# Kernel optimization log

Hardware: AMD Instinct MI355X
Metric: run time of the kernel (lower is better)

## Reference

```python
import jax, jax.numpy as jnp
import numpy as np


def setup_inputs() -> dict:
    key = jax.random.key(0)
    x = jax.random.normal(key, (2, 192, 360, 720), dtype=jnp.float32)
    return {"x": x, "pad_width": 3}


def reference(x, pad_width):
    # x: [B, C, H, W]; geo-cyclic padding:
    #  - circular (periodic) padding of width pad_width in longitude (last axis)
    #  - polar wrap: top/bottom halo rows are rows reflected across the pole,
    #    shifted by half the longitude circle (W // 2).
    B, C, H, W = x.shape
    p = pad_width
    # Circular longitude padding: [B, C, H, W + 2p]
    cp = jnp.concatenate([x[:, :, :, -p:], x, x[:, :, :, :p]], axis=3)
    mid = W // 2
    # Each halo row is cat(row[mid:], row[:mid]) == roll by -mid along longitude.
    rolled = jnp.roll(cp, -mid, axis=3)
    i = np.arange(p)
    top_rows = (p - i - 1) % H          # rows written at output rows 0..p-1
    bottom_rows = (H - i - 1) % H       # rows written at output rows H+p..H+2p-1
    top = rolled[:, :, top_rows, :]     # [B, C, p, W+2p]
    bottom = rolled[:, :, bottom_rows, :]
    # Output: [B, C, H + 2p, W + 2p]
    return jnp.concatenate([top, cp, bottom], axis=2)
```

## Files before the change

kernel.cpp:

```cpp
#include <hip/hip_runtime.h>


typedef float f4u __attribute__((ext_vector_type(4), aligned(4)));
typedef float f2u __attribute__((ext_vector_type(2), aligned(8)));

__global__ __launch_bounds__(256) void geo_pad_kernel(const float* __restrict__ x,
                                                      float* __restrict__ out) {
    constexpr int W = 720, H = 360, p = 3, Wp = 726, Hp = 366;
    constexpr int TPR = 182;

    const unsigned t = blockIdx.x * 256u + threadIdx.x;
    const unsigned row = t / TPR;
    const int j = (int)(t - row * TPR);
    const int ho = (int)(row % Hp);
    const int bc = (int)(row / Hp);

    const bool mid = (ho >= p) & (ho < p + H);
    const int h = mid ? (ho - p) : ((ho < p) ? (p - 1 - ho) : (2 * H + p - 1 - ho));
    const int off = mid ? 0 : (W / 2);

    const float* __restrict__ srow = x + ((size_t)bc * H + h) * W;
    float* __restrict__ orow = out + (size_t)row * Wp;

    if (j < TPR - 1) {
        const int wp0 = 4 * j;
        int wr0 = wp0 + off;      if (wr0 >= Wp) wr0 -= Wp;
        int wr3 = wp0 + 3 + off;  if (wr3 >= Wp) wr3 -= Wp;
        int w0 = wr0 - p; if (w0 < 0) w0 += W; else if (w0 >= W) w0 -= W;
        int w3 = wr3 - p; if (w3 < 0) w3 += W; else if (w3 >= W) w3 -= W;

        float v0, v1, v2, v3;
        if (w3 == w0 + 3) {
            f4u tmp = __builtin_nontemporal_load(
                reinterpret_cast<const f4u*>(srow + w0));
            v0 = tmp.x; v1 = tmp.y; v2 = tmp.z; v3 = tmp.w;
        } else {
            int wr1 = wp0 + 1 + off; if (wr1 >= Wp) wr1 -= Wp;
            int wr2 = wp0 + 2 + off; if (wr2 >= Wp) wr2 -= Wp;
            int w1 = wr1 - p; if (w1 < 0) w1 += W; else if (w1 >= W) w1 -= W;
            int w2 = wr2 - p; if (w2 < 0) w2 += W; else if (w2 >= W) w2 -= W;
            v0 = srow[w0]; v1 = srow[w1]; v2 = srow[w2]; v3 = srow[w3];
        }
        f4u sv; sv.x = v0; sv.y = v1; sv.z = v2; sv.w = v3;
        __builtin_nontemporal_store(sv, reinterpret_cast<f4u*>(orow + wp0));
    } else {
        int wr0 = 724 + off; if (wr0 >= Wp) wr0 -= Wp;
        int w0 = wr0 - p; if (w0 < 0) w0 += W; else if (w0 >= W) w0 -= W;
        f2u sv; sv.x = srow[w0]; sv.y = srow[w0 + 1];
        __builtin_nontemporal_store(sv, reinterpret_cast<f2u*>(orow + 724));
    }
}

extern "C" void kernel_launch(void* const* d_in, const int* in_sizes, int n_in,
                              void* d_out, int out_size, void* d_ws, size_t ws_size,
                              hipStream_t stream) {
    const float* x = (const float*)d_in[0];
    float* out = (float*)d_out;

    const unsigned total = 384u * 366u * 182u;
    const unsigned block = 256;
    const unsigned grid = total / block;

    geo_pad_kernel<<<grid, block, 0, stream>>>(x, out);
}
```

Before: 147.3 us.

## Split padding into aligned-input bulk copy and scalar halo pass

The kernel now maps bulk threads to input rows, so every thread does a 16-byte-aligned vector load of four floats and stores them, offset by the pad, into the interior of the output. A separate set of threads writes the left and right column halos and the polar halo rows one float at a time. This removes the per-thread wrap-around index arithmetic and the scalar fallback path from the interior copy. In exchange, the vector stores are always misaligned, because of the 3-column offset and the 726-float row stride, and the halos use scalar, non-coalesced-friendly accesses.

```diff
diff --git a/kernel.cpp b/kernel.cpp
--- a/kernel.cpp
+++ b/kernel.cpp
@@ -1,53 +1,57 @@
 #include <hip/hip_runtime.h>
 
 
+typedef float f4a __attribute__((ext_vector_type(4), aligned(16)));
 typedef float f4u __attribute__((ext_vector_type(4), aligned(4)));
-typedef float f2u __attribute__((ext_vector_type(2), aligned(8)));
 
 __global__ __launch_bounds__(256) void geo_pad_kernel(const float* __restrict__ x,
                                                       float* __restrict__ out) {
     constexpr int W = 720, H = 360, p = 3, Wp = 726, Hp = 366;
-    constexpr int TPR = 182;
+    constexpr unsigned BULK = 384u * 360u * 180u;
+    constexpr unsigned EPP  = 360u * 6u + 6u * 726u;
 
     const unsigned t = blockIdx.x * 256u + threadIdx.x;
-    const unsigned row = t / TPR;
-    const int j = (int)(t - row * TPR);
-    const int ho = (int)(row % Hp);
-    const int bc = (int)(row / Hp);
 
-    const bool mid = (ho >= p) & (ho < p + H);
-    const int h = mid ? (ho - p) : ((ho < p) ? (p - 1 - ho) : (2 * H + p - 1 - ho));
-    const int off = mid ? 0 : (W / 2);
+    if (t < BULK) {
+        const unsigned k  = t % 180u;
+        const unsigned rr = t / 180u;
+        const unsigned r  = rr % 360u;
+        const unsigned bc = rr / 360u;
 
-    const float* __restrict__ srow = x + ((size_t)bc * H + h) * W;
-    float* __restrict__ orow = out + (size_t)row * Wp;
+        const f4a* src = reinterpret_cast<const f4a*>(
+            x + (size_t)(bc * 360u + r) * W) + k;
+        f4a v = __builtin_nontemporal_load(src);
 
-    if (j < TPR - 1) {
-        const int wp0 = 4 * j;
-        int wr0 = wp0 + off;      if (wr0 >= Wp) wr0 -= Wp;
-        int wr3 = wp0 + 3 + off;  if (wr3 >= Wp) wr3 -= Wp;
-        int w0 = wr0 - p; if (w0 < 0) w0 += W; else if (w0 >= W) w0 -= W;
-        int w3 = wr3 - p; if (w3 < 0) w3 += W; else if (w3 >= W) w3 -= W;
+        float* dst = out + ((size_t)bc * Hp + (r + 3)) * Wp + 3 + 4 * k;
+        f4u sv;
+        sv.x = v.x; sv.y = v.y; sv.z = v.z; sv.w = v.w;
+        __builtin_nontemporal_store(sv, reinterpret_cast<f4u*>(dst));
+    } else {
+        const unsigned e  = t - BULK;
+        const unsigned bc = e / EPP;
+        const unsigned q  = e % EPP;
 
-        float v0, v1, v2, v3;
-        if (w3 == w0 + 3) {
-            f4u tmp = __builtin_nontemporal_load(
-                reinterpret_cast<const f4u*>(srow + w0));
-            v0 = tmp.x; v1 = tmp.y; v2 = tmp.z; v3 = tmp.w;
+        int ho, col, h, w;
+        if (q < 2160u) {
+            const int r  = (int)(q / 6u);
+            const int c6 = (int)(q % 6u);
+            ho  = r + p;
+            h   = r;
+            col = (c6 < 3) ? c6 : (720 + c6);
+            w   = (c6 < 3) ? (717 + c6) : (c6 - 3);
         } else {
-            int wr1 = wp0 + 1 + off; if (wr1 >= Wp) wr1 -= Wp;
-            int wr2 = wp0 + 2 + off; if (wr2 >= Wp) wr2 -= Wp;
-            int w1 = wr1 - p; if (w1 < 0) w1 += W; else if (w1 >= W) w1 -= W;
-            int w2 = wr2 - p; if (w2 < 0) w2 += W; else if (w2 >= W) w2 -= W;
-            v0 = srow[w0]; v1 = srow[w1]; v2 = srow[w2]; v3 = srow[w3];
+            const unsigned q2 = q - 2160u;
+            const int hr = (int)(q2 / (unsigned)Wp);
+            col = (int)(q2 % (unsigned)Wp);
+            ho  = (hr < p) ? hr : (H + hr);
+            h   = (hr < p) ? (p - 1 - hr) : (362 - hr);
+            int wr = col + W / 2;
+            if (wr >= Wp) wr -= Wp;
+            w = wr - p;
+            if (w < 0) w += W; else if (w >= W) w -= W;
         }
-        f4u sv; sv.x = v0; sv.y = v1; sv.z = v2; sv.w = v3;
-        __builtin_nontemporal_store(sv, reinterpret_cast<f4u*>(orow + wp0));
-    } else {
-        int wr0 = 724 + off; if (wr0 >= Wp) wr0 -= Wp;
-        int w0 = wr0 - p; if (w0 < 0) w0 += W; else if (w0 >= W) w0 -= W;
-        f2u sv; sv.x = srow[w0]; sv.y = srow[w0 + 1];
-        __builtin_nontemporal_store(sv, reinterpret_cast<f2u*>(orow + 724));
+        out[((size_t)bc * Hp + ho) * Wp + col] =
+            x[((size_t)bc * H + h) * W + w];
     }
 }
 
@@ -57,9 +61,6 @@
     const float* x = (const float*)d_in[0];
     float* out = (float*)d_out;
 
-    const unsigned total = 384u * 366u * 182u;
-    const unsigned block = 256;
-    const unsigned grid = total / block;
-
-    geo_pad_kernel<<<grid, block, 0, stream>>>(x, out);
+    const unsigned total = 384u * 360u * 180u + 384u * (360u * 6u + 6u * 726u);
+    geo_pad_kernel<<<total / 256u, 256, 0, stream>>>(x, out);
 }
```

Measured after the change: 144.0 us. 1.02x faster.

## Realign interior row loads with wave shuffles and split halo rows into separate blocks

Applied to the files above, without the earlier changes.

Each wavefront now handles one output row. Interior rows use 16-byte-aligned vector loads from the input and rebuild the 3-element shifted output with lane shuffles, plus an extra load for lane 0. This replaces the misaligned per-thread gathers and the per-thread row/column index arithmetic. Polar halo rows go to dedicated trailing blocks that use scalar gathers. The cost is shuffle work, some idle lanes in the third iteration, and 16-byte alignment declared on output rows whose stride is only 8-byte aligned.

```diff
diff --git a/kernel.cpp b/kernel.cpp
--- a/kernel.cpp
+++ b/kernel.cpp
@@ -1,53 +1,89 @@
 #include <hip/hip_runtime.h>
 
 
-typedef float f4u __attribute__((ext_vector_type(4), aligned(4)));
-typedef float f2u __attribute__((ext_vector_type(2), aligned(8)));
+typedef float f4a __attribute__((ext_vector_type(4), aligned(16)));
+typedef float f2a __attribute__((ext_vector_type(2), aligned(8)));
 
 __global__ __launch_bounds__(256) void geo_pad_kernel(const float* __restrict__ x,
                                                       float* __restrict__ out) {
     constexpr int W = 720, H = 360, p = 3, Wp = 726, Hp = 366;
-    constexpr int TPR = 182;
+    constexpr unsigned MIDROWS = 384u * 360u;
+    constexpr unsigned MIDBLK  = MIDROWS / 4u;
 
-    const unsigned t = blockIdx.x * 256u + threadIdx.x;
-    const unsigned row = t / TPR;
-    const int j = (int)(t - row * TPR);
-    const int ho = (int)(row % Hp);
-    const int bc = (int)(row / Hp);
+    const unsigned wid  = threadIdx.x >> 6;
+    const int lane = (int)(threadIdx.x & 63u);
 
-    const bool mid = (ho >= p) & (ho < p + H);
-    const int h = mid ? (ho - p) : ((ho < p) ? (p - 1 - ho) : (2 * H + p - 1 - ho));
-    const int off = mid ? 0 : (W / 2);
+    if (blockIdx.x < MIDBLK) {
+        const unsigned row = blockIdx.x * 4u + wid;
+        const unsigned r  = row % 360u;
+        const unsigned bc = row / 360u;
+        const f4a* __restrict__ sg =
+            reinterpret_cast<const f4a*>(x + (size_t)row * W);
+        float* __restrict__ orow = out + ((size_t)bc * Hp + (r + 3)) * Wp;
 
-    const float* __restrict__ srow = x + ((size_t)bc * H + h) * W;
-    float* __restrict__ orow = out + (size_t)row * Wp;
+#pragma unroll
+        for (int j = 0; j < 3; ++j) {
+            const int g = 64 * j + lane;
+            int gi = g; if (gi >= 180) gi -= 180;
+            f4a cur = __builtin_nontemporal_load(sg + gi);
+            float py = __shfl_up(cur.y, 1);
+            float pz = __shfl_up(cur.z, 1);
+            float pw = __shfl_up(cur.w, 1);
+            if (lane == 0) {
+                const int pgi = (j == 0) ? 179 : (64 * j - 1);
+                f4a pv = *(sg + pgi);
+                py = pv.y; pz = pv.z; pw = pv.w;
+            }
+            if (g < 181) {
+                f4a sv; sv.x = py; sv.y = pz; sv.z = pw; sv.w = cur.x;
+                __builtin_nontemporal_store(sv, reinterpret_cast<f4a*>(orow) + g);
+            } else if (g == 181) {
+                f2a sv; sv.x = py; sv.y = pz;
+                __builtin_nontemporal_store(sv, reinterpret_cast<f2a*>(orow + 724));
+            }
+        }
+    } else {
+        const unsigned hrow = (blockIdx.x - MIDBLK) * 4u + wid;
+        const unsigned hr = hrow % 6u;
+        const unsigned bc = hrow / 6u;
+        const int ho = (hr < 3u) ? (int)hr : (int)(360u + hr);
+        const int h  = (hr < 3u) ? (int)(2u - hr) : (int)(362u - hr);
+        const float* __restrict__ srow = x + ((size_t)bc * H + h) * W;
+        float* __restrict__ orow = out + ((size_t)bc * Hp + ho) * Wp;
 
-    if (j < TPR - 1) {
-        const int wp0 = 4 * j;
-        int wr0 = wp0 + off;      if (wr0 >= Wp) wr0 -= Wp;
-        int wr3 = wp0 + 3 + off;  if (wr3 >= Wp) wr3 -= Wp;
-        int w0 = wr0 - p; if (w0 < 0) w0 += W; else if (w0 >= W) w0 -= W;
-        int w3 = wr3 - p; if (w3 < 0) w3 += W; else if (w3 >= W) w3 -= W;
-
-        float v0, v1, v2, v3;
-        if (w3 == w0 + 3) {
-            f4u tmp = __builtin_nontemporal_load(
-                reinterpret_cast<const f4u*>(srow + w0));
-            v0 = tmp.x; v1 = tmp.y; v2 = tmp.z; v3 = tmp.w;
-        } else {
-            int wr1 = wp0 + 1 + off; if (wr1 >= Wp) wr1 -= Wp;
-            int wr2 = wp0 + 2 + off; if (wr2 >= Wp) wr2 -= Wp;
-            int w1 = wr1 - p; if (w1 < 0) w1 += W; else if (w1 >= W) w1 -= W;
-            int w2 = wr2 - p; if (w2 < 0) w2 += W; else if (w2 >= W) w2 -= W;
-            v0 = srow[w0]; v1 = srow[w1]; v2 = srow[w2]; v3 = srow[w3];
+#pragma unroll
+        for (int j = 0; j < 3; ++j) {
+            const int g = 64 * j + lane;
+            const int c0 = 4 * g;
+            float v0, v1, v2, v3;
+            {
+                int wr = c0 + 360;     if (wr >= Wp) wr -= Wp;
+                int w  = wr - p; if (w < 0) w += W; else if (w >= W) w -= W;
+                v0 = srow[w];
+            }
+            {
+                int wr = c0 + 361;     if (wr >= Wp) wr -= Wp;
+                int w  = wr - p; if (w < 0) w += W; else if (w >= W) w -= W;
+                v1 = srow[w];
+            }
+            {
+                int wr = c0 + 362;     if (wr >= Wp) wr -= Wp;
+                int w  = wr - p; if (w < 0) w += W; else if (w >= W) w -= W;
+                v2 = srow[w];
+            }
+            {
+                int wr = c0 + 363;     if (wr >= Wp) wr -= Wp;
+                int w  = wr - p; if (w < 0) w += W; else if (w >= W) w -= W;
+                v3 = srow[w];
+            }
+            if (g < 181) {
+                f4a sv; sv.x = v0; sv.y = v1; sv.z = v2; sv.w = v3;
+                __builtin_nontemporal_store(sv, reinterpret_cast<f4a*>(orow) + g);
+            } else if (g == 181) {
+                f2a sv; sv.x = v0; sv.y = v1;
+                __builtin_nontemporal_store(sv, reinterpret_cast<f2a*>(orow + 724));
+            }
         }
-        f4u sv; sv.x = v0; sv.y = v1; sv.z = v2; sv.w = v3;
-        __builtin_nontemporal_store(sv, reinterpret_cast<f4u*>(orow + wp0));
-    } else {
-        int wr0 = 724 + off; if (wr0 >= Wp) wr0 -= Wp;
-        int w0 = wr0 - p; if (w0 < 0) w0 += W; else if (w0 >= W) w0 -= W;
-        f2u sv; sv.x = srow[w0]; sv.y = srow[w0 + 1];
-        __builtin_nontemporal_store(sv, reinterpret_cast<f2u*>(orow + 724));
     }
 }
 
@@ -57,9 +93,6 @@
     const float* x = (const float*)d_in[0];
     float* out = (float*)d_out;
 
-    const unsigned total = 384u * 366u * 182u;
-    const unsigned block = 256;
-    const unsigned grid = total / block;
-
-    geo_pad_kernel<<<grid, block, 0, stream>>>(x, out);
+    const unsigned grid = 34560u + 576u;
+    geo_pad_kernel<<<grid, 256, 0, stream>>>(x, out);
 }
```

Result: slower. 166.7 us (+13.2%).
